# Performance work log

Hardware: AMD Instinct MI355X
Metric: run time of the kernel (lower is better)

Reference implementation:

```python
import jax, jax.numpy as jnp
import numpy as np


def setup_inputs() -> dict:
    key = jax.random.key(0)
    B, N, F = 32, 8192, 256
    x = jax.random.normal(key, (B, N, F), dtype=jnp.float32)
    return {"x": x, "k": 1024}


def reference(x, k):
    # Sort rows of each graph by last feature, descending, keep top k.
    # Original: per-batch argsort(desc) + gather, then truncate to k (N > k here).
    # lax.top_k returns indices of the k largest values in descending order,
    # equivalent to argsort(desc)[:k] without a full sort.
    _, idx = jax.lax.top_k(x[..., -1], k)          # idx: [B, k]
    out = jnp.take_along_axis(x, idx[:, :, None], axis=1)  # [B, k, F]
    return out
```

## Files before the change

kernel.cpp:

```cpp
#include <hip/hip_runtime.h>
#include <hip/hip_bf16.h>

#define B_DIM 32
#define N_DIM 8192
#define F_DIM 256
#define K_DIM 1024
#define RUNS_PER_B 8

__device__ __forceinline__ unsigned int f32_ord(float v) {
    unsigned int u = __float_as_uint(v);
    return (u & 0x80000000u) ? ~u : (u | 0x80000000u);
}

__global__ __launch_bounds__(512)
void sort_runs_kernel(const float* __restrict__ x,
                      unsigned long long* __restrict__ runs) {
    __shared__ unsigned long long K[K_DIM];

    const int blk = blockIdx.x;
    const int b   = blk >> 3;
    const int c   = blk & 7;
    const float* xcol = x + (size_t)b * N_DIM * F_DIM + (F_DIM - 1);
    const int base = c * K_DIM;

    for (int i = threadIdx.x; i < K_DIM; i += 512) {
        int row = base + i;
        float v = xcol[(size_t)row * F_DIM];
        K[i] = ((unsigned long long)f32_ord(v) << 32) |
               (unsigned int)(N_DIM - 1 - row);
    }
    __syncthreads();

    for (unsigned int kk = 2; kk <= K_DIM; kk <<= 1) {
        for (unsigned int jj = kk >> 1; jj > 0; jj >>= 1) {
            unsigned int p = threadIdx.x;
            unsigned int i = ((p & ~(jj - 1)) << 1) | (p & (jj - 1));
            unsigned int j = i | jj;
            unsigned long long a  = K[i];
            unsigned long long bb = K[j];
            bool desc = ((i & kk) == 0);
            if (desc ? (a < bb) : (a > bb)) { K[i] = bb; K[j] = a; }
            __syncthreads();
        }
    }

    ulonglong2* dst = (ulonglong2*)(runs + (size_t)blk * K_DIM);
    const ulonglong2* src = (const ulonglong2*)K;
    dst[threadIdx.x] = src[threadIdx.x];
}

__global__ __launch_bounds__(1024)
void merge_topk_kernel(const unsigned long long* __restrict__ runs,
                       int* __restrict__ idx_out) {
    __shared__ unsigned long long K[N_DIM];

    const int b = blockIdx.x;
    const ulonglong2* src = (const ulonglong2*)(runs + (size_t)b * N_DIM);
    ulonglong2* Kv = (ulonglong2*)K;
    for (unsigned int i = threadIdx.x; i < N_DIM / 2; i += 1024) Kv[i] = src[i];
    __syncthreads();

    for (int level = 0; level < 3; ++level) {
        const unsigned int m      = 4u >> level;
        const unsigned int stride = 1024u << level;
        const unsigned int shift  = 11 + level;

        for (unsigned int t = threadIdx.x; t < m * 1024u; t += 1024) {
            unsigned int g = t >> 10, i = t & 1023u;
            unsigned int a = g << shift;
            unsigned long long bv = K[a + stride + 1023u - i];
            if (bv > K[a + i]) K[a + i] = bv;
        }
        __syncthreads();

        for (unsigned int jj = 512; jj > 0; jj >>= 1) {
            for (unsigned int t = threadIdx.x; t < m * 512u; t += 1024) {
                unsigned int g = t >> 9, p = t & 511u;
                unsigned int base = g << shift;
                unsigned int i = base + (((p & ~(jj - 1)) << 1) | (p & (jj - 1)));
                unsigned int j = i | jj;
                unsigned long long a = K[i];
                unsigned long long c = K[j];
                if (a < c) { K[i] = c; K[j] = a; }
            }
            __syncthreads();
        }
    }

    for (unsigned int i = threadIdx.x; i < K_DIM; i += 1024) {
        unsigned int low = (unsigned int)(K[i] & 0xFFFFFFFFu);
        idx_out[b * K_DIM + i] = (int)(N_DIM - 1 - low);
    }
}

__global__ __launch_bounds__(256)
void gather_rows_kernel(const float* __restrict__ x,
                        const int* __restrict__ idx,
                        float* __restrict__ out) {
    size_t gid = (size_t)blockIdx.x * blockDim.x + threadIdx.x;
    int f4     = (int)(gid & (F_DIM / 4 - 1));
    size_t row = gid >> 6;
    int b      = (int)(row >> 10);
    int src    = idx[row];

    const float4* src_ptr =
        (const float4*)(x + ((size_t)b * N_DIM + (size_t)src) * F_DIM) + f4;
    ((float4*)out)[gid] = *src_ptr;
}

extern "C" void kernel_launch(void* const* d_in, const int* in_sizes, int n_in,
                              void* d_out, int out_size, void* d_ws, size_t ws_size,
                              hipStream_t stream) {
    const float* x = (const float*)d_in[0];
    float* out = (float*)d_out;

    unsigned long long* runs = (unsigned long long*)d_ws;
    int* idx_ws = (int*)((char*)d_ws + (size_t)B_DIM * N_DIM * 8);

    sort_runs_kernel<<<B_DIM * RUNS_PER_B, 512, 0, stream>>>(x, runs);
    merge_topk_kernel<<<B_DIM, 1024, 0, stream>>>(runs, idx_ws);

    const size_t total_f4 = (size_t)B_DIM * K_DIM * F_DIM / 4;
    gather_rows_kernel<<<(int)(total_f4 / 256), 256, 0, stream>>>(x, idx_ws, out);
}
```

Baseline: 343.5 us.

## Reduce each 4096-row chunk to top-1024 inside the sort kernel

After: 360.5 us. 1.05x slower.

```diff
diff --git a/kernel.cpp b/kernel.cpp
--- a/kernel.cpp
+++ b/kernel.cpp
@@ -5,25 +5,26 @@
 #define N_DIM 8192
 #define F_DIM 256
 #define K_DIM 1024
-#define RUNS_PER_B 8
+#define CHUNK 4096
+#define CHUNKS_PER_B 2
 
 __device__ __forceinline__ unsigned int f32_ord(float v) {
     unsigned int u = __float_as_uint(v);
     return (u & 0x80000000u) ? ~u : (u | 0x80000000u);
 }
 
-__global__ __launch_bounds__(512)
-void sort_runs_kernel(const float* __restrict__ x,
-                      unsigned long long* __restrict__ runs) {
-    __shared__ unsigned long long K[K_DIM];
+__global__ __launch_bounds__(1024)
+void sort_chunks_kernel(const float* __restrict__ x,
+                        unsigned long long* __restrict__ runs) {
+    __shared__ unsigned long long K[CHUNK];
 
     const int blk = blockIdx.x;
-    const int b   = blk >> 3;
-    const int c   = blk & 7;
+    const int b   = blk >> 1;
+    const int c   = blk & 1;
     const float* xcol = x + (size_t)b * N_DIM * F_DIM + (F_DIM - 1);
-    const int base = c * K_DIM;
+    const int base = c * CHUNK;
 
-    for (int i = threadIdx.x; i < K_DIM; i += 512) {
+    for (int i = threadIdx.x; i < CHUNK; i += 1024) {
         int row = base + i;
         float v = xcol[(size_t)row * F_DIM];
         K[i] = ((unsigned long long)f32_ord(v) << 32) |
@@ -31,64 +32,100 @@
     }
     __syncthreads();
 
-    for (unsigned int kk = 2; kk <= K_DIM; kk <<= 1) {
+    for (unsigned int kk = 2; kk <= 1024; kk <<= 1) {
         for (unsigned int jj = kk >> 1; jj > 0; jj >>= 1) {
-            unsigned int p = threadIdx.x;
-            unsigned int i = ((p & ~(jj - 1)) << 1) | (p & (jj - 1));
-            unsigned int j = i | jj;
-            unsigned long long a  = K[i];
-            unsigned long long bb = K[j];
-            bool desc = ((i & kk) == 0);
-            if (desc ? (a < bb) : (a > bb)) { K[i] = bb; K[j] = a; }
-            __syncthreads();
-        }
-    }
-
-    ulonglong2* dst = (ulonglong2*)(runs + (size_t)blk * K_DIM);
-    const ulonglong2* src = (const ulonglong2*)K;
-    dst[threadIdx.x] = src[threadIdx.x];
-}
-
-__global__ __launch_bounds__(1024)
-void merge_topk_kernel(const unsigned long long* __restrict__ runs,
-                       int* __restrict__ idx_out) {
-    __shared__ unsigned long long K[N_DIM];
-
-    const int b = blockIdx.x;
-    const ulonglong2* src = (const ulonglong2*)(runs + (size_t)b * N_DIM);
-    ulonglong2* Kv = (ulonglong2*)K;
-    for (unsigned int i = threadIdx.x; i < N_DIM / 2; i += 1024) Kv[i] = src[i];
-    __syncthreads();
-
-    for (int level = 0; level < 3; ++level) {
-        const unsigned int m      = 4u >> level;
-        const unsigned int stride = 1024u << level;
-        const unsigned int shift  = 11 + level;
-
-        for (unsigned int t = threadIdx.x; t < m * 1024u; t += 1024) {
-            unsigned int g = t >> 10, i = t & 1023u;
-            unsigned int a = g << shift;
-            unsigned long long bv = K[a + stride + 1023u - i];
-            if (bv > K[a + i]) K[a + i] = bv;
-        }
-        __syncthreads();
-
-        for (unsigned int jj = 512; jj > 0; jj >>= 1) {
-            for (unsigned int t = threadIdx.x; t < m * 512u; t += 1024) {
-                unsigned int g = t >> 9, p = t & 511u;
-                unsigned int base = g << shift;
-                unsigned int i = base + (((p & ~(jj - 1)) << 1) | (p & (jj - 1)));
-                unsigned int j = i | jj;
-                unsigned long long a = K[i];
-                unsigned long long c = K[j];
-                if (a < c) { K[i] = c; K[j] = a; }
+            for (unsigned int p = threadIdx.x; p < 2048; p += 1024) {
+                unsigned int q  = p >> 9;
+                unsigned int lp = p & 511u;
+                unsigned int il = ((lp & ~(jj - 1)) << 1) | (lp & (jj - 1));
+                unsigned int i  = (q << 10) + il;
+                unsigned int j  = i | jj;
+                bool desc = (((il & kk) == 0) != (bool)(q & 1));
+                unsigned long long a  = K[i];
+                unsigned long long bb = K[j];
+                if (desc ? (a < bb) : (a > bb)) { K[i] = bb; K[j] = a; }
             }
             __syncthreads();
         }
     }
 
-    for (unsigned int i = threadIdx.x; i < K_DIM; i += 1024) {
-        unsigned int low = (unsigned int)(K[i] & 0xFFFFFFFFu);
+    for (unsigned int t = threadIdx.x; t < 2048; t += 1024) {
+        unsigned int h = t >> 10, i = t & 1023u;
+        unsigned int a = h << 11;
+        unsigned long long bv = K[a + 1024u + i];
+        if (bv > K[a + i]) K[a + i] = bv;
+    }
+    __syncthreads();
+
+    for (unsigned int jj = 512; jj > 0; jj >>= 1) {
+        unsigned int p  = threadIdx.x;
+        unsigned int h  = p >> 9;
+        unsigned int lp = p & 511u;
+        unsigned int il = ((lp & ~(jj - 1)) << 1) | (lp & (jj - 1));
+        unsigned int i  = (h << 11) + il;
+        unsigned int j  = i | jj;
+        bool desc = (h == 0);
+        unsigned long long a  = K[i];
+        unsigned long long bb = K[j];
+        if (desc ? (a < bb) : (a > bb)) { K[i] = bb; K[j] = a; }
+        __syncthreads();
+    }
+
+    if (threadIdx.x < 1024) {
+        unsigned int i = threadIdx.x;
+        unsigned long long bv = K[2048u + i];
+        if (bv > K[i]) K[i] = bv;
+    }
+    __syncthreads();
+
+    for (unsigned int jj = 512; jj > 0; jj >>= 1) {
+        if (threadIdx.x < 512) {
+            unsigned int lp = threadIdx.x;
+            unsigned int i = ((lp & ~(jj - 1)) << 1) | (lp & (jj - 1));
+            unsigned int j = i | jj;
+            unsigned long long a  = K[i];
+            unsigned long long bb = K[j];
+            if (a < bb) { K[i] = bb; K[j] = a; }
+        }
+        __syncthreads();
+    }
+
+    if (threadIdx.x < 512) {
+        ulonglong2* dst = (ulonglong2*)(runs + (size_t)blk * K_DIM);
+        const ulonglong2* srcv = (const ulonglong2*)K;
+        dst[threadIdx.x] = srcv[threadIdx.x];
+    }
+}
+
+__global__ __launch_bounds__(512)
+void merge_topk_kernel(const unsigned long long* __restrict__ runs,
+                       int* __restrict__ idx_out) {
+    __shared__ unsigned long long A[2 * K_DIM];
+
+    const int b = blockIdx.x;
+    const ulonglong2* src = (const ulonglong2*)(runs + (size_t)b * 2 * K_DIM);
+    ulonglong2* Av = (ulonglong2*)A;
+    for (unsigned int i = threadIdx.x; i < K_DIM; i += 512) Av[i] = src[i];
+    __syncthreads();
+
+    for (unsigned int i = threadIdx.x; i < K_DIM; i += 512) {
+        unsigned long long bv = A[2047u - i];
+        if (bv > A[i]) A[i] = bv;
+    }
+    __syncthreads();
+
+    for (unsigned int jj = 512; jj > 0; jj >>= 1) {
+        unsigned int lp = threadIdx.x;
+        unsigned int i = ((lp & ~(jj - 1)) << 1) | (lp & (jj - 1));
+        unsigned int j = i | jj;
+        unsigned long long a = A[i];
+        unsigned long long c = A[j];
+        if (a < c) { A[i] = c; A[j] = a; }
+        __syncthreads();
+    }
+
+    for (unsigned int i = threadIdx.x; i < K_DIM; i += 512) {
+        unsigned int low = (unsigned int)(A[i] & 0xFFFFFFFFu);
         idx_out[b * K_DIM + i] = (int)(N_DIM - 1 - low);
     }
 }
@@ -115,10 +152,10 @@
     float* out = (float*)d_out;
 
     unsigned long long* runs = (unsigned long long*)d_ws;
-    int* idx_ws = (int*)((char*)d_ws + (size_t)B_DIM * N_DIM * 8);
+    int* idx_ws = (int*)((char*)d_ws + (size_t)B_DIM * CHUNKS_PER_B * K_DIM * 8);
 
-    sort_runs_kernel<<<B_DIM * RUNS_PER_B, 512, 0, stream>>>(x, runs);
-    merge_topk_kernel<<<B_DIM, 1024, 0, stream>>>(runs, idx_ws);
+    sort_chunks_kernel<<<B_DIM * CHUNKS_PER_B, 1024, 0, stream>>>(x, runs);
+    merge_topk_kernel<<<B_DIM, 512, 0, stream>>>(runs, idx_ws);
 
     const size_t total_f4 = (size_t)B_DIM * K_DIM * F_DIM / 4;
     gather_rows_kernel<<<(int)(total_f4 / 256), 256, 0, stream>>>(x, idx_ws, out);
```
